# Kernel tuning notes

Measured on AMD Instinct MI355X. Metric: run time of the kernel, lower is better.

Reference implementation:

```python
import jax, jax.numpy as jnp
import numpy as np

D_MODEL = 768
HEAD = 12
D_K = D_MODEL // HEAD


def setup_inputs() -> dict:
    key = jax.random.key(0)
    ks = jax.random.split(key, 9)
    s = 1.0 / np.sqrt(D_MODEL)
    return {
        "x": jax.random.normal(ks[0], (2, 4096, D_MODEL), dtype=jnp.float32),
        "Wq": jax.random.normal(ks[1], (D_MODEL, D_MODEL), dtype=jnp.float32) * s,
        "bq": jax.random.normal(ks[2], (D_MODEL,), dtype=jnp.float32) * 0.01,
        "Wk": jax.random.normal(ks[3], (D_MODEL, D_MODEL), dtype=jnp.float32) * s,
        "bk": jax.random.normal(ks[4], (D_MODEL,), dtype=jnp.float32) * 0.01,
        "Wv": jax.random.normal(ks[5], (D_MODEL, D_MODEL), dtype=jnp.float32) * s,
        "bv": jax.random.normal(ks[6], (D_MODEL,), dtype=jnp.float32) * 0.01,
        "Wo": jax.random.normal(ks[7], (D_MODEL, D_MODEL), dtype=jnp.float32) * s,
        "bo": jax.random.normal(ks[8], (D_MODEL,), dtype=jnp.float32) * 0.01,
    }


def reference(x, Wq, bq, Wk, bk, Wv, bv, Wo, bo):
    B, S, _ = x.shape
    # Linear projections, split into heads: [B, H, S, d_k]
    def proj(W, b):
        return (x @ W + b).reshape(B, S, HEAD, D_K).transpose(0, 2, 1, 3)
    Q, K, V = proj(Wq, bq), proj(Wk, bk), proj(Wv, bv)
    scale = 1.0 / jnp.sqrt(jnp.asarray(D_K, x.dtype))
    # [B, H, S, S] attention scores (materialized, as in the original module)
    scores = jnp.einsum('bhqd,bhkd->bhqk', Q, K) * scale
    probs = jax.nn.softmax(scores, axis=-1)  # dropout is identity in eval mode
    ctx = jnp.einsum('bhqk,bhkd->bhqd', probs, V)
    ctx = ctx.transpose(0, 2, 1, 3).reshape(B, S, D_MODEL)
    return ctx @ Wo + bo
```

## Files before the change

kernel.cpp:

```cpp
#include <hip/hip_runtime.h>

#define D_MODEL 768
#define S_LEN   4096
#define NHEAD   12
#define DK      64
#define TKA     64

typedef _Float16 f16;
typedef _Float16 f16x8 __attribute__((ext_vector_type(8)));
typedef _Float16 f16x4 __attribute__((ext_vector_type(4)));
typedef __fp16   fp16x2 __attribute__((ext_vector_type(2)));
typedef float    f32x4 __attribute__((ext_vector_type(4)));
typedef float    f32x2 __attribute__((ext_vector_type(2)));

#define MFMA16(a, b, c) __builtin_amdgcn_mfma_f32_16x16x32_f16(a, b, c, 0, 0, 0)

#define Q_PRESCALE 0.18033688f
#define SOFTMAX_C  11.54156036f

__device__ inline f16x8 ldf(const f16* p) {
    return *reinterpret_cast<const f16x8*>(p);
}

__device__ inline void gl2lds16(const f16* g, f16* l) {
    __builtin_amdgcn_global_load_lds(
        (const __attribute__((address_space(1))) void*)g,
        (__attribute__((address_space(3))) void*)l, 16, 0, 0);
}

__global__ __launch_bounds__(256) void cvt_x_kernel(const float* __restrict__ x,
                                                    f16* __restrict__ xb) {
    size_t i = ((size_t)blockIdx.x * 256 + threadIdx.x) * 4;
    float4 v = *reinterpret_cast<const float4*>(x + i);
    f16x4 o = { (f16)v.x, (f16)v.y, (f16)v.z, (f16)v.w };
    *reinterpret_cast<f16x4*>(xb + i) = o;
}

__global__ __launch_bounds__(256) void wtrans_kernel(const float* __restrict__ Wq,
                                                     const float* __restrict__ Wk,
                                                     const float* __restrict__ Wv,
                                                     const float* __restrict__ Wo,
                                                     f16* __restrict__ WT) {
    const int z = blockIdx.z;
    const float* in = (z == 0) ? Wq : (z == 1) ? Wk : (z == 2) ? Wv : Wo;
    f16* out = WT + (size_t)z * D_MODEL * D_MODEL;
    __shared__ float tile[32][33];
    const int tx = threadIdx.x, ty = threadIdx.y;
    const int n0 = blockIdx.x * 32, k0 = blockIdx.y * 32;
#pragma unroll
    for (int j = 0; j < 32; j += 8)
        tile[ty + j][tx] = in[(size_t)(k0 + ty + j) * D_MODEL + n0 + tx];
    __syncthreads();
#pragma unroll
    for (int j = 0; j < 32; j += 8)
        out[(size_t)(n0 + ty + j) * D_MODEL + k0 + tx] = (f16)tile[tx][ty + j];
}

__global__ __launch_bounds__(256, 3) void gemm_qkv_kernel(
        const f16* __restrict__ A, const f16* __restrict__ WT,
        const float* __restrict__ bq, const float* __restrict__ bk,
        const float* __restrict__ bv,
        f16* __restrict__ Qb, f16* __restrict__ Kb, f16* __restrict__ Vt) {
    __shared__ __align__(16) f16 asmem[3][128 * 32];
    __shared__ __align__(16) f16 bsmem[3][128 * 32];
    const int z = blockIdx.z;
    const f16* Bt = WT + (size_t)z * D_MODEL * D_MODEL;
    const float* bias = (z == 0) ? bq : (z == 1) ? bk : bv;
    const int w = threadIdx.x >> 6;
    const int lane = threadIdx.x & 63;
    const int ln = lane & 15, quad = lane >> 4;
    const int mb = blockIdx.x * 128;
    const int nb = blockIdx.y * 128;
    const int mloc = (w & 1) * 64, nloc = (w >> 1) * 64;
    const int l0 = w * 64 + lane;

    auto stage = [&](int buf, int kb) {
#pragma unroll
        for (int p = 0; p < 2; p++) {
            const int l = p * 256 + l0;
            gl2lds16(A + (size_t)(mb + (l >> 2)) * D_MODEL + kb + (l & 3) * 8,
                     &asmem[buf][(p * 256 + w * 64) * 8]);
        }
#pragma unroll
        for (int p = 0; p < 2; p++) {
            const int l = p * 256 + l0;
            gl2lds16(Bt + (size_t)(nb + (l >> 2)) * D_MODEL + kb + (l & 3) * 8,
                     &bsmem[buf][(p * 256 + w * 64) * 8]);
        }
    };

    f32x4 acc[4][4] = {};
    stage(0, 0);
    stage(1, 32);
    __syncthreads();

    const int NIT = D_MODEL / 32;
    int cb = 0, sb = 2;
    for (int it = 0; it < NIT; ++it) {
        f16x8 af[4], bf[4];
#pragma unroll
        for (int i = 0; i < 4; i++)
            af[i] = ldf(&asmem[cb][(mloc + i * 16 + ln) * 32 + quad * 8]);
#pragma unroll
        for (int t = 0; t < 4; t++)
            bf[t] = ldf(&bsmem[cb][(nloc + t * 16 + ln) * 32 + quad * 8]);
#pragma unroll
        for (int i = 0; i < 4; i++)
#pragma unroll
            for (int t = 0; t < 4; t++)
                acc[i][t] = MFMA16(af[i], bf[t], acc[i][t]);
        __syncthreads();
        if (it + 2 < NIT) stage(sb, (it + 2) * 32);
        cb = (cb == 2) ? 0 : cb + 1;
        sb = (sb == 2) ? 0 : sb + 1;
    }

#pragma unroll
    for (int t = 0; t < 4; t++) {
        const int n = nb + nloc + t * 16 + ln;
        const float bval = bias[n];
        const int h = n >> 6, d = n & 63;
#pragma unroll
        for (int i = 0; i < 4; i++) {
            const int m = mb + mloc + i * 16 + quad * 4;
            const int b = m >> 12, s = m & 4095;
            const int bh = b * NHEAD + h;
            if (z == 0) {
#pragma unroll
                for (int r = 0; r < 4; r++)
                    Qb[((size_t)bh * S_LEN + s + r) * DK + d] =
                        (f16)((acc[i][t][r] + bval) * Q_PRESCALE);
            } else if (z == 1) {
#pragma unroll
                for (int r = 0; r < 4; r++)
                    Kb[((size_t)bh * S_LEN + s + r) * DK + d] =
                        (f16)(acc[i][t][r] + bval);
            } else {
                f16x4 pk;
#pragma unroll
                for (int r = 0; r < 4; r++) pk[r] = (f16)(acc[i][t][r] + bval);
                *reinterpret_cast<f16x4*>(&Vt[((size_t)bh * DK + d) * S_LEN + s]) = pk;
            }
        }
    }
}

__global__ __launch_bounds__(256, 3) void attn_kernel(const f16* __restrict__ Qb,
                                                      const f16* __restrict__ Kb,
                                                      const f16* __restrict__ Vt,
                                                      f16* __restrict__ Ctx) {
    __shared__ __align__(16) f16 kbuf[3][TKA * DK];
    __shared__ __align__(16) f16 vbuf[3][DK * TKA];

    const int w = threadIdx.x >> 6;
    const int lane = threadIdx.x & 63;
    const int ln = lane & 15, quad = lane >> 4;

    const int blk = blockIdx.x;
    const int xcd = blk & 7, sidx = blk >> 3;
    const int bh = xcd * 3 + (sidx >> 5);
    const int qb = (sidx & 31) * 128;
    const int b = bh / NHEAD, h = bh % NHEAD;

    const f16* Kbh = Kb + (size_t)bh * S_LEN * DK;
    const f16* Vbh = Vt + (size_t)bh * DK * S_LEN;

    f16x8 aq[2][2];
#pragma unroll
    for (int i2 = 0; i2 < 2; i2++) {
        const f16* qp = Qb + ((size_t)bh * S_LEN + qb + w * 32 + i2 * 16 + ln) * DK;
        aq[i2][0] = ldf(qp + quad * 8);
        aq[i2][1] = ldf(qp + 32 + quad * 8);
    }

    int rS[2], ckS[2], cvS[2];
#pragma unroll
    for (int p = 0; p < 2; p++) {
        const int l = p * 256 + w * 64 + lane;
        const int r = l >> 3;
        rS[p]  = r;
        ckS[p] = ((l & 7) - r - (r >> 2)) & 7;
        cvS[p] = ((l & 7) - r - (r >> 3)) & 7;
    }

    auto stage = [&](int buf, int kk) {
#pragma unroll
        for (int p = 0; p < 2; p++)
            gl2lds16(Kbh + (size_t)(kk + rS[p]) * DK + ckS[p] * 8,
                     &kbuf[buf][(p * 256 + w * 64) * 8]);
#pragma unroll
        for (int p = 0; p < 2; p++)
            gl2lds16(Vbh + (size_t)rS[p] * S_LEN + kk + cvS[p] * 8,
                     &vbuf[buf][(p * 256 + w * 64) * 8]);
    };

    int koff[2][2][2];
#pragma unroll
    for (int kt = 0; kt < 2; kt++)
#pragma unroll
        for (int a = 0; a < 2; a++) {
            const int rr = kt * 32 + 8 * (ln >> 2) + 4 * a + (ln & 3);
            const int sw = rr + (rr >> 2);
            koff[kt][a][0] = rr * DK + (((quad + sw) & 7) * 8);
            koff[kt][a][1] = rr * DK + (((quad + 4 + sw) & 7) * 8);
        }
    int voff[4][2];
#pragma unroll
    for (int t = 0; t < 4; t++) {
        const int rr = t * 16 + ln;
        const int sw = rr + (rr >> 3);
#pragma unroll
        for (int kt = 0; kt < 2; kt++)
            voff[t][kt] = rr * TKA + (((quad + 4 * kt + sw) & 7) * 8);
    }

    const f32x4 cinit = { -SOFTMAX_C, -SOFTMAX_C, -SOFTMAX_C, -SOFTMAX_C };
    f32x4 acc[4][2] = {};
    f32x2 lsum2[2] = {};

    stage(0, 0);
    stage(1, TKA);
    __syncthreads();

    const int NIT = S_LEN / TKA;
    int cb = 0, sb = 2;
    for (int it = 0; it < NIT; ++it) {
        const f16* kb = kbuf[cb];
        const f16* vb = vbuf[cb];

        union { f16x8 v; fp16x2 h2[4]; } pb[2][2];

#pragma unroll
        for (int kt = 0; kt < 2; kt++) {
#pragma unroll
            for (int a = 0; a < 2; a++) {
                const f16x8 kf0 = ldf(kb + koff[kt][a][0]);
                const f16x8 kf1 = ldf(kb + koff[kt][a][1]);
#pragma unroll
                for (int i2 = 0; i2 < 2; i2++) {
                    f32x4 si = MFMA16(kf0, aq[i2][0], cinit);
                    si = MFMA16(kf1, aq[i2][1], si);
                    const float e0 = __builtin_amdgcn_exp2f(si[0]);
                    const float e1 = __builtin_amdgcn_exp2f(si[1]);
                    const float e2 = __builtin_amdgcn_exp2f(si[2]);
                    const float e3 = __builtin_amdgcn_exp2f(si[3]);
                    f32x2 ea = { e0, e1 };
                    f32x2 eb = { e2, e3 };
                    lsum2[i2] += ea + eb;
                    pb[kt][i2].h2[2 * a]     = __builtin_amdgcn_cvt_pkrtz(e0, e1);
                    pb[kt][i2].h2[2 * a + 1] = __builtin_amdgcn_cvt_pkrtz(e2, e3);
                }
            }
        }

        __builtin_amdgcn_s_setprio(1);
#pragma unroll
        for (int t = 0; t < 4; t++) {
#pragma unroll
            for (int kt = 0; kt < 2; kt++) {
                const f16x8 vf = ldf(vb + voff[t][kt]);
#pragma unroll
                for (int i2 = 0; i2 < 2; i2++)
                    acc[t][i2] = MFMA16(vf, pb[kt][i2].v, acc[t][i2]);
            }
        }
        __builtin_amdgcn_s_setprio(0);

        __syncthreads();
        if (it + 2 < NIT) stage(sb, (it + 2) * TKA);
        cb = (cb == 2) ? 0 : cb + 1;
        sb = (sb == 2) ? 0 : sb + 1;
    }

#pragma unroll
    for (int i2 = 0; i2 < 2; i2++) {
        float l = lsum2[i2][0] + lsum2[i2][1];
        l += __shfl_xor(l, 16, 64);
        l += __shfl_xor(l, 32, 64);
        const float rl = 1.0f / l;
        const int q = qb + w * 32 + i2 * 16 + ln;
        f16* cp = Ctx + ((size_t)b * S_LEN + q) * D_MODEL + h * DK + 4 * quad;
#pragma unroll
        for (int t = 0; t < 4; t++) {
            f16x4 pk;
#pragma unroll
            for (int r = 0; r < 4; r++) pk[r] = (f16)(acc[t][i2][r] * rl);
            *reinterpret_cast<f16x4*>(cp + t * 16) = pk;
        }
    }
}

__global__ __launch_bounds__(256, 3) void gemm_o_kernel(const f16* __restrict__ A,
                                                        const f16* __restrict__ Bt,
                                                        const float* __restrict__ bo,
                                                        float* __restrict__ out) {
    __shared__ __align__(16) f16 asmem[3][64 * 32];
    __shared__ __align__(16) f16 bsmem[3][128 * 32];
    const int w = threadIdx.x >> 6;
    const int lane = threadIdx.x & 63;
    const int ln = lane & 15, quad = lane >> 4;
    const int mb = blockIdx.x * 64;
    const int nb = blockIdx.y * 128;
    const int mloc = (w & 1) * 32, nloc = (w >> 1) * 64;
    const int l0 = w * 64 + lane;

    auto stage = [&](int buf, int kb) {
        gl2lds16(A + (size_t)(mb + (l0 >> 2)) * D_MODEL + kb + (l0 & 3) * 8,
                 &asmem[buf][(w * 64) * 8]);
#pragma unroll
        for (int p = 0; p < 2; p++) {
            const int l = p * 256 + l0;
            gl2lds16(Bt + (size_t)(nb + (l >> 2)) * D_MODEL + kb + (l & 3) * 8,
                     &bsmem[buf][(p * 256 + w * 64) * 8]);
        }
    };

    f32x4 acc[2][4] = {};
    stage(0, 0);
    stage(1, 32);
    __syncthreads();

    const int NIT = D_MODEL / 32;
    int cb = 0, sb = 2;
    for (int it = 0; it < NIT; ++it) {
        f16x8 af[2], bf[4];
#pragma unroll
        for (int i = 0; i < 2; i++)
            af[i] = ldf(&asmem[cb][(mloc + i * 16 + ln) * 32 + quad * 8]);
#pragma unroll
        for (int t = 0; t < 4; t++)
            bf[t] = ldf(&bsmem[cb][(nloc + t * 16 + ln) * 32 + quad * 8]);
#pragma unroll
        for (int i = 0; i < 2; i++)
#pragma unroll
            for (int t = 0; t < 4; t++)
                acc[i][t] = MFMA16(af[i], bf[t], acc[i][t]);
        __syncthreads();
        if (it + 2 < NIT) stage(sb, (it + 2) * 32);
        cb = (cb == 2) ? 0 : cb + 1;
        sb = (sb == 2) ? 0 : sb + 1;
    }

#pragma unroll
    for (int t = 0; t < 4; t++) {
        const int n = nb + nloc + t * 16 + ln;
        const float bval = bo[n];
#pragma unroll
        for (int i = 0; i < 2; i++) {
            const int m = mb + mloc + i * 16 + quad * 4;
#pragma unroll
            for (int r = 0; r < 4; r++)
                out[(size_t)(m + r) * D_MODEL + n] = acc[i][t][r] + bval;
        }
    }
}

extern "C" void kernel_launch(void* const* d_in, const int* in_sizes, int n_in,
                              void* d_out, int out_size, void* d_ws, size_t ws_size,
                              hipStream_t stream) {
    const float* x  = (const float*)d_in[0];
    const float* Wq = (const float*)d_in[1];
    const float* bq = (const float*)d_in[2];
    const float* Wk = (const float*)d_in[3];
    const float* bk = (const float*)d_in[4];
    const float* Wv = (const float*)d_in[5];
    const float* bv = (const float*)d_in[6];
    const float* Wo = (const float*)d_in[7];
    const float* bo = (const float*)d_in[8];
    float* out = (float*)d_out;

    f16* ws = (f16*)d_ws;
    f16* Xb  = ws;
    f16* Ctx = ws;
    f16* WT  = ws + 6291456;
    f16* Qb  = ws + 8650752;
    f16* Kb  = ws + 14942208;
    f16* Vt  = ws + 21233664;

    cvt_x_kernel<<<6144, 256, 0, stream>>>(x, Xb);
    wtrans_kernel<<<dim3(24, 24, 4), dim3(32, 8), 0, stream>>>(Wq, Wk, Wv, Wo, WT);
    gemm_qkv_kernel<<<dim3(64, 6, 3), 256, 0, stream>>>(Xb, WT, bq, bk, bv, Qb, Kb, Vt);
    attn_kernel<<<768, 256, 0, stream>>>(Qb, Kb, Vt, Ctx);
    gemm_o_kernel<<<dim3(128, 6), 256, 0, stream>>>(Ctx, WT + (size_t)3 * D_MODEL * D_MODEL, bo, out);
}
```

Baseline: 274.2 us.

## Switch QKV GEMM to double-buffered LDS with unrolled pair loop and hoisted addresses

The QKV projection GEMM goes from a three-stage LDS ring to two buffers, with the main loop unrolled by two so buffer indices are compile-time constants. Global source pointers and LDS fragment offsets are precomputed once outside the loop, and the occupancy hint rises from 3 to 4 blocks per CU. The aim is to cut index arithmetic and LDS footprint so more blocks fit per CU. In exchange, prefetch distance is shorter: after each sync the next stage is issued into the buffer just consumed, which may expose global load latency.

```diff
diff --git a/kernel.cpp b/kernel.cpp
--- a/kernel.cpp
+++ b/kernel.cpp
@@ -56,13 +56,13 @@
         out[(size_t)(n0 + ty + j) * D_MODEL + k0 + tx] = (f16)tile[tx][ty + j];
 }
 
-__global__ __launch_bounds__(256, 3) void gemm_qkv_kernel(
+__global__ __launch_bounds__(256, 4) void gemm_qkv_kernel(
         const f16* __restrict__ A, const f16* __restrict__ WT,
         const float* __restrict__ bq, const float* __restrict__ bk,
         const float* __restrict__ bv,
         f16* __restrict__ Qb, f16* __restrict__ Kb, f16* __restrict__ Vt) {
-    __shared__ __align__(16) f16 asmem[3][128 * 32];
-    __shared__ __align__(16) f16 bsmem[3][128 * 32];
+    __shared__ __align__(16) f16 asmem[2][128 * 32];
+    __shared__ __align__(16) f16 bsmem[2][128 * 32];
     const int z = blockIdx.z;
     const f16* Bt = WT + (size_t)z * D_MODEL * D_MODEL;
     const float* bias = (z == 0) ? bq : (z == 1) ? bk : bv;
@@ -74,45 +74,55 @@
     const int mloc = (w & 1) * 64, nloc = (w >> 1) * 64;
     const int l0 = w * 64 + lane;
 
+    const f16* aS[2];
+    const f16* bS[2];
+#pragma unroll
+    for (int p = 0; p < 2; p++) {
+        const int l = p * 256 + l0;
+        aS[p] = A  + (size_t)(mb + (l >> 2)) * D_MODEL + (l & 3) * 8;
+        bS[p] = Bt + (size_t)(nb + (l >> 2)) * D_MODEL + (l & 3) * 8;
+    }
     auto stage = [&](int buf, int kb) {
 #pragma unroll
-        for (int p = 0; p < 2; p++) {
-            const int l = p * 256 + l0;
-            gl2lds16(A + (size_t)(mb + (l >> 2)) * D_MODEL + kb + (l & 3) * 8,
-                     &asmem[buf][(p * 256 + w * 64) * 8]);
-        }
-#pragma unroll
-        for (int p = 0; p < 2; p++) {
-            const int l = p * 256 + l0;
-            gl2lds16(Bt + (size_t)(nb + (l >> 2)) * D_MODEL + kb + (l & 3) * 8,
-                     &bsmem[buf][(p * 256 + w * 64) * 8]);
-        }
+        for (int p = 0; p < 2; p++)
+            gl2lds16(aS[p] + kb, &asmem[buf][(p * 256 + w * 64) * 8]);
+#pragma unroll
+        for (int p = 0; p < 2; p++)
+            gl2lds16(bS[p] + kb, &bsmem[buf][(p * 256 + w * 64) * 8]);
     };
 
+    int aoff[4], boff[4];
+#pragma unroll
+    for (int i = 0; i < 4; i++) aoff[i] = (mloc + i * 16 + ln) * 32 + quad * 8;
+#pragma unroll
+    for (int t = 0; t < 4; t++) boff[t] = (nloc + t * 16 + ln) * 32 + quad * 8;
+
     f32x4 acc[4][4] = {};
+    auto body = [&](const f16* as, const f16* bs) {
+        f16x8 af[4], bf[4];
+#pragma unroll
+        for (int i = 0; i < 4; i++) af[i] = ldf(as + aoff[i]);
+#pragma unroll
+        for (int t = 0; t < 4; t++) bf[t] = ldf(bs + boff[t]);
+#pragma unroll
+        for (int i = 0; i < 4; i++)
+#pragma unroll
+            for (int t = 0; t < 4; t++)
+                acc[i][t] = MFMA16(af[i], bf[t], acc[i][t]);
+    };
+
     stage(0, 0);
     stage(1, 32);
     __syncthreads();
 
-    const int NIT = D_MODEL / 32;
-    int cb = 0, sb = 2;
-    for (int it = 0; it < NIT; ++it) {
-        f16x8 af[4], bf[4];
-#pragma unroll
-        for (int i = 0; i < 4; i++)
-            af[i] = ldf(&asmem[cb][(mloc + i * 16 + ln) * 32 + quad * 8]);
-#pragma unroll
-        for (int t = 0; t < 4; t++)
-            bf[t] = ldf(&bsmem[cb][(nloc + t * 16 + ln) * 32 + quad * 8]);
-#pragma unroll
-        for (int i = 0; i < 4; i++)
-#pragma unroll
-            for (int t = 0; t < 4; t++)
-                acc[i][t] = MFMA16(af[i], bf[t], acc[i][t]);
+#pragma unroll 1
+    for (int j = 0; j < 12; ++j) {
+        body(asmem[0], bsmem[0]);
         __syncthreads();
-        if (it + 2 < NIT) stage(sb, (it + 2) * 32);
-        cb = (cb == 2) ? 0 : cb + 1;
-        sb = (sb == 2) ? 0 : sb + 1;
+        if (j < 11) stage(0, (2 * j + 2) * 32);
+        body(asmem[1], bsmem[1]);
+        __syncthreads();
+        if (j < 11) stage(1, (2 * j + 3) * 32);
     }
 
 #pragma unroll
```

Measured after the change: 281.2 us. 1.03x slower.
